# Kernel tuning notes

Hardware: AMD Instinct MI355X
Metric: run time of the kernel (lower is better)

## Reference

```python
import jax, jax.numpy as jnp
import numpy as np
import math

V, D, H, L, DFF = 32000, 1024, 16, 4, 4096
B, T_TGT, T_SRC = 4, 512, 512


def setup_inputs() -> dict:
    key = jax.random.key(0)
    ks = iter(jax.random.split(key, 64))
    s = 0.02
    inp = {
        'tgt': jax.random.randint(next(ks), (B, T_TGT), 0, V, dtype=jnp.int32),
        'encoder_output': jax.random.normal(next(ks), (B, T_SRC, D), jnp.float32),
        'tgt_mask': jnp.tril(jnp.ones((T_TGT, T_TGT), jnp.int32)),
        'emb': jax.random.normal(next(ks), (V, D)) * s,
        'Wout': jax.random.normal(next(ks), (D, V)) * s,
        'bout': jnp.zeros((V,)),
    }
    for pfx in ('s', 'c'):  # self / cross attention
        for nm in ('q', 'k', 'v', 'o'):
            inp[f'W{nm}_{pfx}'] = jax.random.normal(next(ks), (L, D, D)) * s
            inp[f'b{nm}_{pfx}'] = jnp.zeros((L, D))
    inp['W1'] = jax.random.normal(next(ks), (L, D, DFF)) * s
    inp['b1'] = jnp.zeros((L, DFF))
    inp['W2'] = jax.random.normal(next(ks), (L, DFF, D)) * s
    inp['b2'] = jnp.zeros((L, D))
    for i in (1, 2, 3):
        inp[f'ln{i}_g'] = jnp.ones((L, D))
        inp[f'ln{i}_b'] = jnp.zeros((L, D))
    return inp


def _layernorm(x, g, b, eps=1e-5):
    m = x.mean(-1, keepdims=True)
    v = ((x - m) ** 2).mean(-1, keepdims=True)
    return g * (x - m) * jax.lax.rsqrt(v + eps) + b


def _mha(xq, xkv, Wq, bq, Wk, bk, Wv, bv, Wo, bo, mask):
    Bq, Tq, Dm = xq.shape
    dk = Dm // H
    q = (xq @ Wq + bq).reshape(Bq, Tq, H, dk).transpose(0, 2, 1, 3)   # bhqd
    k = (xkv @ Wk + bk).reshape(Bq, -1, H, dk).transpose(0, 2, 1, 3)  # bhkd
    v = (xkv @ Wv + bv).reshape(Bq, -1, H, dk).transpose(0, 2, 1, 3)
    scores = jnp.einsum('bhqd,bhkd->bhqk', q, k) / math.sqrt(dk)
    if mask is not None:
        scores = jnp.where(mask[None, None] == 0, -1e9, scores)
    w = jax.nn.softmax(scores, axis=-1)                               # dropout: eval mode
    o = jnp.einsum('bhqk,bhkd->bhqd', w, v).transpose(0, 2, 1, 3).reshape(Bq, Tq, Dm)
    return o @ Wo + bo, w


def _pos_encoding(T, Dm):
    pos = jnp.arange(T, dtype=jnp.float32)[:, None]
    div = jnp.exp(jnp.arange(0, Dm, 2, dtype=jnp.float32) * (-math.log(10000.0) / Dm))
    pe = jnp.zeros((T, Dm))
    pe = pe.at[:, 0::2].set(jnp.sin(pos * div))
    pe = pe.at[:, 1::2].set(jnp.cos(pos * div))
    return pe


def reference(tgt, encoder_output, tgt_mask, emb, Wout, bout,
              Wq_s, bq_s, Wk_s, bk_s, Wv_s, bv_s, Wo_s, bo_s,
              Wq_c, bq_c, Wk_c, bk_c, Wv_c, bv_c, Wo_c, bo_c,
              W1, b1, W2, b2, ln1_g, ln1_b, ln2_g, ln2_b, ln3_g, ln3_b):
    x = emb[tgt] * math.sqrt(D) + _pos_encoding(tgt.shape[1], D)[None]
    self_ws, cross_ws = [], []
    for i in range(L):
        a1, sw = _mha(x, x, Wq_s[i], bq_s[i], Wk_s[i], bk_s[i], Wv_s[i], bv_s[i],
                      Wo_s[i], bo_s[i], tgt_mask)
        x = _layernorm(x + a1, ln1_g[i], ln1_b[i])
        a2, cw = _mha(x, encoder_output, Wq_c[i], bq_c[i], Wk_c[i], bk_c[i],
                      Wv_c[i], bv_c[i], Wo_c[i], bo_c[i], None)
        x = _layernorm(x + a2, ln2_g[i], ln2_b[i])
        ffn = jax.nn.relu(x @ W1[i] + b1[i]) @ W2[i] + b2[i]
        x = _layernorm(x + ffn, ln3_g[i], ln3_b[i])
        self_ws.append(sw)
        cross_ws.append(cw)
    logits = x @ Wout + bout
    return logits, jnp.stack(self_ws), jnp.stack(cross_ws)
```

## Files before the change

kernel.cpp:

```cpp
#include <hip/hip_runtime.h>


typedef unsigned short u16;
typedef __bf16 v8bf __attribute__((ext_vector_type(8)));
typedef float v4f __attribute__((ext_vector_type(4)));

namespace {
constexpr int kB = 4, kT = 512, kD = 1024, kH = 16, kDK = 64, kF = 4096, kV = 32000, kL = 4;
constexpr int kM = kB * kT;
constexpr long kTD = (long)kT * kD;
constexpr long kTT = (long)kT * kT;
constexpr long kHTT = (long)kH * kTT;
constexpr long kBHTT = (long)kB * kHTT;
constexpr long kLOG = (long)kM * kV;
constexpr long kPART = (long)kM * kD;
}

__device__ __forceinline__ u16 f2bf(float f) {
  union { float f; unsigned u; } v; v.f = f;
  unsigned r = v.u + 0x7FFFu + ((v.u >> 16) & 1u);
  return (u16)(r >> 16);
}
__device__ __forceinline__ float bf2f(u16 h) {
  union { unsigned u; float f; } v; v.u = ((unsigned)h) << 16;
  return v.f;
}

typedef __attribute__((address_space(3))) void lds_void;
typedef const __attribute__((address_space(1))) void glob_void;
__device__ __forceinline__ void gl2lds16(const void* g, void* l) {
  __builtin_amdgcn_global_load_lds((glob_void*)g, (lds_void*)l, 16, 0, 0);
}

template <int BM, int BN, int OUTBF, int VTR, int DBUF>
__global__ __launch_bounds__(256)
void gemm_bf(const u16* __restrict__ A0, const u16* __restrict__ B0,
             const float* __restrict__ bias, void* __restrict__ Cv,
             u16* __restrict__ vtw,
             const int K, const int lda, const int ldb, const int ldc,
             const int nH, const long sAb, const long sAh,
             const long sBb, const long sBh, const long sCb, const long sCh,
             const float scale, const int relu, const int bstride) {
  static_assert(BM % 32 == 0 && BN % 32 == 0, "tiles");
  __shared__ u16 As[DBUF + 1][BM][64];
  __shared__ u16 Bs[DBUF + 1][BN][64];
  const int tid = threadIdx.x;
  const int lane = tid & 63;
  const int w = tid >> 6;
  const int z = blockIdx.z;
  const int zb = z / nH, zh = z - zb * nH;
  const u16* A = A0 + zb * sAb + zh * sAh + (long)blockIdx.y * BM * lda;
  const u16* B = B0 + zb * sBb + zh * sBh + (long)blockIdx.x * BN * ldb;
  const long offC = zb * sCb + zh * sCh;
  const int wm = w >> 1, wn = w & 1;
  constexpr int FM = BM / 32, FN = BN / 32;
  v4f acc[FM][FN];
  const v4f zero = {0.f, 0.f, 0.f, 0.f};
#pragma unroll
  for (int i = 0; i < FM; ++i)
#pragma unroll
    for (int j = 0; j < FN; ++j) acc[i][j] = zero;
  const int l15 = lane & 15, lk = lane >> 4;
  const int lr8 = lane >> 3;
  const int swz = ((lane & 7) ^ lr8) * 8;
  const int l7 = l15 & 7;

  if constexpr (DBUF) {
#pragma unroll
    for (int s = 0; s < BM / 32; ++s)
      gl2lds16(A + (long)(w * (BM / 4) + s * 8 + lr8) * lda + swz,
               &As[0][w * (BM / 4) + s * 8][0]);
#pragma unroll
    for (int s = 0; s < BN / 32; ++s)
      gl2lds16(B + (long)(w * (BN / 4) + s * 8 + lr8) * ldb + swz,
               &Bs[0][w * (BN / 4) + s * 8][0]);

    const int NT = K >> 6;
    for (int kt = 0; kt < NT; ++kt) {
      const int cur = kt & 1;
      __syncthreads();
      if (kt + 1 < NT) {
        const int k0 = (kt + 1) << 6;
#pragma unroll
        for (int s = 0; s < BM / 32; ++s)
          gl2lds16(A + (long)(w * (BM / 4) + s * 8 + lr8) * lda + k0 + swz,
                   &As[cur ^ 1][w * (BM / 4) + s * 8][0]);
#pragma unroll
        for (int s = 0; s < BN / 32; ++s)
          gl2lds16(B + (long)(w * (BN / 4) + s * 8 + lr8) * ldb + k0 + swz,
                   &Bs[cur ^ 1][w * (BN / 4) + s * 8][0]);
      }
#pragma unroll
      for (int t = 0; t < 2; ++t) {
        const int c0 = t * 4;
        v8bf af[FM], bfr[FN];
#pragma unroll
        for (int i = 0; i < FM; ++i)
          af[i] = *(const v8bf*)&As[cur][wm * (BM / 2) + i * 16 + l15][((c0 + lk) ^ l7) * 8];
#pragma unroll
        for (int j = 0; j < FN; ++j)
          bfr[j] = *(const v8bf*)&Bs[cur][wn * (BN / 2) + j * 16 + l15][((c0 + lk) ^ l7) * 8];
#pragma unroll
        for (int i = 0; i < FM; ++i)
#pragma unroll
          for (int j = 0; j < FN; ++j)
            acc[i][j] = __builtin_amdgcn_mfma_f32_16x16x32_bf16(af[i], bfr[j], acc[i][j], 0, 0, 0);
      }
    }
  } else {
    for (int k0 = 0; k0 < K; k0 += 64) {
      __syncthreads();
#pragma unroll
      for (int s = 0; s < BM / 32; ++s)
        gl2lds16(A + (long)(w * (BM / 4) + s * 8 + lr8) * lda + k0 + swz,
                 &As[0][w * (BM / 4) + s * 8][0]);
#pragma unroll
      for (int s = 0; s < BN / 32; ++s)
        gl2lds16(B + (long)(w * (BN / 4) + s * 8 + lr8) * ldb + k0 + swz,
                 &Bs[0][w * (BN / 4) + s * 8][0]);
      __syncthreads();
#pragma unroll
      for (int t = 0; t < 2; ++t) {
        const int c0 = t * 4;
        v8bf af[FM], bfr[FN];
#pragma unroll
        for (int i = 0; i < FM; ++i)
          af[i] = *(const v8bf*)&As[0][wm * (BM / 2) + i * 16 + l15][((c0 + lk) ^ l7) * 8];
#pragma unroll
        for (int j = 0; j < FN; ++j)
          bfr[j] = *(const v8bf*)&Bs[0][wn * (BN / 2) + j * 16 + l15][((c0 + lk) ^ l7) * 8];
#pragma unroll
        for (int i = 0; i < FM; ++i)
#pragma unroll
          for (int j = 0; j < FN; ++j)
            acc[i][j] = __builtin_amdgcn_mfma_f32_16x16x32_bf16(af[i], bfr[j], acc[i][j], 0, 0, 0);
      }
    }
  }

  const long m0 = (long)blockIdx.y * BM + wm * (BM / 2);
  const int n0 = blockIdx.x * BN + wn * (BN / 2);
#pragma unroll
  for (int j = 0; j < FN; ++j) {
    const int col = n0 + j * 16 + l15;
    const float bv = (bias && zb == 0) ? bias[zh * bstride + col] : 0.0f;
#pragma unroll
    for (int i = 0; i < FM; ++i) {
      const long row = m0 + i * 16 + lk * 4;
#pragma unroll
      for (int r = 0; r < 4; ++r) {
        float v = acc[i][j][r] * scale + bv;
        if (relu) v = fmaxf(v, 0.0f);
        const long idx = offC + (row + r) * ldc + col;
        if (OUTBF) ((u16*)Cv)[idx] = f2bf(v);
        else       ((float*)Cv)[idx] = v;
        if (VTR) {
          const int colS = (int)(offC % 3072) + col;
          if (colS >= 2048) {
            const int hh = (colS - 2048) >> 6, dd = (colS - 2048) & 63;
            const int rowg = (int)(row + r);
            vtw[((long)((rowg >> 9) * 16 + hh)) * 32768 + dd * 512 + (rowg & 511)] = f2bf(v);
          }
        }
      }
    }
  }
}

template <int CAUSAL>
__global__ __launch_bounds__(512)
void attn_fused(const u16* __restrict__ Qb, const u16* __restrict__ Kb,
                const u16* __restrict__ vtp, float* __restrict__ wout,
                u16* __restrict__ oout) {
  __shared__ __align__(16) char lds[81920];
  u16 (*Qs)[64] = (u16 (*)[64])lds;
  u16 (*Ks)[64] = (u16 (*)[64])(lds + 16384);
  u16 (*Pl)[136] = (u16 (*)[136])lds;
  u16 (*Vt)[136] = (u16 (*)[136])(lds + 34816);
  __shared__ float redM[128][4];
  __shared__ float redS[128][4];
  const int tid = threadIdx.x, lane = tid & 63, w = tid >> 6;
  const int wm = w >> 2, wn = w & 3;
  const int l15 = lane & 15, lk = lane >> 4;
  const int lr8 = lane >> 3;
  const int swz = ((lane & 7) ^ lr8) * 8;
  const int l7 = l15 & 7;
  const int bx = blockIdx.x;
  const int z = blockIdx.y, zb = z >> 4, zh = z & 15;
  const u16* Q = Qb + (long)zb * 512 * 3072 + zh * 64 + (long)bx * 128 * 3072;
  const u16* Kp = Kb + (long)zb * 512 * 3072 + zh * 64;
  const u16* vtz = vtp + (long)((zb << 4) + zh) * 32768;
  const long obase = (long)zb * kHTT + (long)zh * kTT;

#pragma unroll
  for (int s = 0; s < 2; ++s)
    gl2lds16(Q + (long)(w * 16 + s * 8 + lr8) * 3072 + swz, &Qs[w * 16 + s * 8][0]);
#pragma unroll
  for (int s = 0; s < 8; ++s) {
    const int r0 = w * 64 + s * 8;
    if (!CAUSAL || r0 <= bx * 128 + 127)
      gl2lds16(Kp + (long)(r0 + lr8) * 3072 + swz, &Ks[r0][0]);
  }
  __syncthreads();

  v4f acc[4][8];
  const v4f zero = {0.f, 0.f, 0.f, 0.f};
#pragma unroll
  for (int i = 0; i < 4; ++i)
#pragma unroll
    for (int j = 0; j < 8; ++j) acc[i][j] = zero;

#pragma unroll
  for (int t = 0; t < 2; ++t) {
    const int c0 = t * 4;
    v8bf aq[4], bk[8];
#pragma unroll
    for (int i = 0; i < 4; ++i)
      aq[i] = *(const v8bf*)&Qs[wm * 64 + i * 16 + l15][((c0 + lk) ^ l7) * 8];
#pragma unroll
    for (int j = 0; j < 8; ++j)
      bk[j] = *(const v8bf*)&Ks[wn * 128 + j * 16 + l15][((c0 + lk) ^ l7) * 8];
#pragma unroll
    for (int i = 0; i < 4; ++i)
#pragma unroll
      for (int j = 0; j < 8; ++j)
        if (!(CAUSAL && wn * 128 + j * 16 > bx * 128 + wm * 64 + i * 16 + 15))
          acc[i][j] = __builtin_amdgcn_mfma_f32_16x16x32_bf16(aq[i], bk[j], acc[i][j], 0, 0, 0);
  }

  float gmax[4][4];
#pragma unroll
  for (int i = 0; i < 4; ++i)
#pragma unroll
    for (int r = 0; r < 4; ++r) {
      const int q = bx * 128 + wm * 64 + i * 16 + lk * 4 + r;
      float m = -3.0e38f;
#pragma unroll
      for (int j = 0; j < 8; ++j) {
        const int col = wn * 128 + j * 16 + l15;
        if (!CAUSAL || col <= q) m = fmaxf(m, acc[i][j][r] * 0.125f);
      }
#pragma unroll
      for (int off = 1; off < 16; off <<= 1) m = fmaxf(m, __shfl_xor(m, off));
      if (l15 == 0) redM[wm * 64 + i * 16 + lk * 4 + r][wn] = m;
    }
  __syncthreads();
#pragma unroll
  for (int i = 0; i < 4; ++i)
#pragma unroll
    for (int r = 0; r < 4; ++r) {
      v4f mv = *(const v4f*)&redM[wm * 64 + i * 16 + lk * 4 + r][0];
      gmax[i][r] = fmaxf(fmaxf(mv[0], mv[1]), fmaxf(mv[2], mv[3]));
    }
#pragma unroll
  for (int i = 0; i < 4; ++i)
#pragma unroll
    for (int r = 0; r < 4; ++r) {
      const int q = bx * 128 + wm * 64 + i * 16 + lk * 4 + r;
      float s = 0.0f;
#pragma unroll
      for (int j = 0; j < 8; ++j) {
        const int col = wn * 128 + j * 16 + l15;
        float e = (!CAUSAL || col <= q) ? __expf(acc[i][j][r] * 0.125f - gmax[i][r]) : 0.0f;
        acc[i][j][r] = e;
        s += e;
      }
#pragma unroll
      for (int off = 1; off < 16; off <<= 1) s += __shfl_xor(s, off);
      if (l15 == 0) redS[wm * 64 + i * 16 + lk * 4 + r][wn] = s;
    }
  __syncthreads();
#pragma unroll
  for (int i = 0; i < 4; ++i)
#pragma unroll
    for (int r = 0; r < 4; ++r) {
      v4f sv = *(const v4f*)&redS[wm * 64 + i * 16 + lk * 4 + r][0];
      const float inv = 1.0f / (sv[0] + sv[1] + sv[2] + sv[3]);
      const int q = bx * 128 + wm * 64 + i * 16 + lk * 4 + r;
      const long rowoff = obase + (long)q * 512;
#pragma unroll
      for (int j = 0; j < 8; ++j) {
        const int col = wn * 128 + j * 16 + l15;
        const float v = acc[i][j][r] * inv;
        acc[i][j][r] = v;
        wout[rowoff + col] = v;
      }
    }

  v4f acco[4];
#pragma unroll
  for (int i = 0; i < 4; ++i) acco[i] = zero;
  const int kcMax = CAUSAL ? bx : 3;
  for (int kc = 0; kc <= kcMax; ++kc) {
    __syncthreads();
    if (wn == kc) {
#pragma unroll
      for (int i = 0; i < 4; ++i)
#pragma unroll
        for (int j = 0; j < 8; ++j) {
          const int colk = j * 16 + l15;
#pragma unroll
          for (int r = 0; r < 4; ++r)
            Pl[wm * 64 + i * 16 + lk * 4 + r][colk] = f2bf(acc[i][j][r]);
        }
    }
#pragma unroll
    for (int s = 0; s < 2; ++s) {
      const int c = tid * 2 + s;
      const int d = c >> 4, off = (c & 15) * 8;
      uint4 vv = *(const uint4*)(vtz + (long)d * 512 + kc * 128 + off);
      *(uint4*)&Vt[d][off] = vv;
    }
    __syncthreads();
#pragma unroll
    for (int t = 0; t < 4; ++t) {
      v8bf bv = *(const v8bf*)&Vt[wn * 16 + l15][t * 32 + lk * 8];
#pragma unroll
      for (int i = 0; i < 4; ++i) {
        v8bf ap = *(const v8bf*)&Pl[wm * 64 + i * 16 + l15][t * 32 + lk * 8];
        acco[i] = __builtin_amdgcn_mfma_f32_16x16x32_bf16(ap, bv, acco[i], 0, 0, 0);
      }
    }
  }
#pragma unroll
  for (int i = 0; i < 4; ++i)
#pragma unroll
    for (int r = 0; r < 4; ++r) {
      const int row = bx * 128 + wm * 64 + i * 16 + lk * 4 + r;
      oout[(long)(zb * 512 + row) * 1024 + zh * 64 + wn * 16 + l15] = f2bf(acco[i][r]);
    }
}

struct TPtrs { const float* in[8]; u16* out[8]; };

__global__ void transpose_wt_v3(TPtrs ps, int K, int N) {
  __shared__ float tile[64][65];
  const float* in = ps.in[blockIdx.z];
  u16* o = ps.out[blockIdx.z];
  const int n0 = blockIdx.x * 64, k0 = blockIdx.y * 64;
  const int tr = threadIdx.x >> 4;
  const int tc = (threadIdx.x & 15) * 4;
#pragma unroll
  for (int i = 0; i < 4; ++i) {
    float4 v = *(const float4*)(in + (long)(k0 + tr + 16 * i) * N + n0 + tc);
    tile[tr + 16 * i][tc + 0] = v.x;
    tile[tr + 16 * i][tc + 1] = v.y;
    tile[tr + 16 * i][tc + 2] = v.z;
    tile[tr + 16 * i][tc + 3] = v.w;
  }
  __syncthreads();
#pragma unroll
  for (int i = 0; i < 4; ++i) {
    const int rr = tr + 16 * i;
    u16 h[4];
#pragma unroll
    for (int j = 0; j < 4; ++j) h[j] = f2bf(tile[tc + j][rr]);
    *(uint2*)(o + (long)(n0 + rr) * K + k0 + tc) = *(const uint2*)h;
  }
}

__global__ void concat_bias(float* __restrict__ dst, const float* __restrict__ s0,
                            const float* __restrict__ s1, const float* __restrict__ s2,
                            const int nsrc) {
  const int idx = blockIdx.x * 256 + threadIdx.x;
  const int per = nsrc << 10;
  const int l = idx / per, rem = idx - l * per, s = rem >> 10, j = rem & 1023;
  const float* src = (s == 0) ? s0 : (s == 1 ? s1 : s2);
  dst[idx] = src[l * 1024 + j];
}

__global__ void cvt_bf16_v3(const float* __restrict__ in, u16* __restrict__ o1,
                            u16* __restrict__ o2) {
  const long i = ((long)blockIdx.x * 256 + threadIdx.x) * 4;
  float4 v = *(const float4*)(in + i);
  u16 h[4] = {f2bf(v.x), f2bf(v.y), f2bf(v.z), f2bf(v.w)};
  *(uint2*)(o1 + i) = *(const uint2*)h;
  *(uint2*)(o2 + i) = *(const uint2*)h;
}

__global__ void embed_v2(const int* __restrict__ tgt, const float* __restrict__ emb,
                         float* __restrict__ x, u16* __restrict__ xb) {
  const int row = blockIdx.x;
  const int t = row & (kT - 1);
  const int tok = tgt[row];
  const int c = threadIdx.x * 4;
  float4 e = *(const float4*)(emb + (long)tok * kD + c);
  const float nl = -9.210340371976184f / (float)kD;
  const float a0 = (float)t * expf((float)c * nl);
  const float a1 = (float)t * expf((float)(c + 2) * nl);
  float4 o;
  o.x = e.x * 32.0f + sinf(a0);
  o.y = e.y * 32.0f + cosf(a0);
  o.z = e.z * 32.0f + sinf(a1);
  o.w = e.w * 32.0f + cosf(a1);
  *(float4*)(x + (long)row * kD + c) = o;
  u16 h[4] = {f2bf(o.x), f2bf(o.y), f2bf(o.z), f2bf(o.w)};
  *(uint2*)(xb + (long)row * kD + c) = *(const uint2*)h;
}

__global__ void add_ln_v3(float* __restrict__ x, u16* __restrict__ xb,
                          const float* __restrict__ res, const int nres,
                          const float* __restrict__ g, const float* __restrict__ b) {
  const int row = blockIdx.x;
  const int c = threadIdx.x * 4;
  float4 xv = *(const float4*)(x + (long)row * kD + c);
  float v0 = xv.x, v1 = xv.y, v2 = xv.z, v3 = xv.w;
  for (int p = 0; p < nres; ++p) {
    float4 rv = *(const float4*)(res + p * kPART + (long)row * kD + c);
    v0 += rv.x; v1 += rv.y; v2 += rv.z; v3 += rv.w;
  }
  float s = v0 + v1 + v2 + v3;
  float ss = v0 * v0 + v1 * v1 + v2 * v2 + v3 * v3;
#pragma unroll
  for (int o = 32; o > 0; o >>= 1) { s += __shfl_xor(s, o); ss += __shfl_xor(ss, o); }
  __shared__ float red[4][2];
  const int wv = threadIdx.x >> 6;
  if ((threadIdx.x & 63) == 0) { red[wv][0] = s; red[wv][1] = ss; }
  __syncthreads();
  s  = red[0][0] + red[1][0] + red[2][0] + red[3][0];
  ss = red[0][1] + red[1][1] + red[2][1] + red[3][1];
  const float mean = s * (1.0f / kD);
  const float var = ss * (1.0f / kD) - mean * mean;
  const float rs = rsqrtf(var + 1e-5f);
  float4 gv = *(const float4*)(g + c);
  float4 bv = *(const float4*)(b + c);
  float4 o;
  o.x = gv.x * (v0 - mean) * rs + bv.x;
  o.y = gv.y * (v1 - mean) * rs + bv.y;
  o.z = gv.z * (v2 - mean) * rs + bv.z;
  o.w = gv.w * (v3 - mean) * rs + bv.w;
  *(float4*)(x + (long)row * kD + c) = o;
  u16 h[4] = {f2bf(o.x), f2bf(o.y), f2bf(o.z), f2bf(o.w)};
  *(uint2*)(xb + (long)row * kD + c) = *(const uint2*)h;
}

template <int BM, int BN, typename TA, typename TB, int BKN>
__global__ __launch_bounds__(256)
void gemm_kernel(const void* __restrict__ Av, const void* __restrict__ Bv,
                 const float* __restrict__ bias, float* __restrict__ Cv,
                 const int K, const int lda, const int ldb, const int ldc,
                 const int nH, const long sAb, const long sAh,
                 const long sBb, const long sBh, const long sCb, const long sCh,
                 const float scale, const int relu) {
  constexpr int LP = 40;
  __shared__ u16 As[BM][LP];
  __shared__ u16 Bs[BN][LP];
  const int tid = threadIdx.x;
  const int z = blockIdx.z;
  const int zb = z / nH, zh = z - zb * nH;
  const TA* A = (const TA*)Av + zb * sAb + zh * sAh + (long)blockIdx.y * BM * lda;
  const TB* Bp;
  if constexpr (BKN)
    Bp = (const TB*)Bv + zb * sBb + zh * sBh + (long)blockIdx.x * BN;
  else
    Bp = (const TB*)Bv + zb * sBb + zh * sBh + (long)blockIdx.x * BN * ldb;
  const long offC = zb * sCb + zh * sCh;
  const int lane = tid & 63;
  const int wm = (tid >> 7) & 1, wn = (tid >> 6) & 1;
  constexpr int FM = BM / 32, FN = BN / 32;
  v4f acc[FM][FN];
  const v4f zero = {0.f, 0.f, 0.f, 0.f};
#pragma unroll
  for (int i = 0; i < FM; ++i)
#pragma unroll
    for (int j = 0; j < FN; ++j) acc[i][j] = zero;
  const int l15 = lane & 15, lk = lane >> 4;

  for (int k0 = 0; k0 < K; k0 += 32) {
    __syncthreads();
    if constexpr (sizeof(TA) == 4) {
      const int r = tid >> 3, c = (tid & 7) * 4;
#pragma unroll
      for (int rr = 0; rr < BM; rr += 32) {
        float4 vv = *(const float4*)((const float*)A + (long)(rr + r) * lda + k0 + c);
        unsigned lo = (unsigned)f2bf(vv.x) | ((unsigned)f2bf(vv.y) << 16);
        unsigned hi = (unsigned)f2bf(vv.z) | ((unsigned)f2bf(vv.w) << 16);
        *(uint2*)&As[rr + r][c] = make_uint2(lo, hi);
      }
    } else {
      const int r = tid >> 2, c = (tid & 3) * 8;
#pragma unroll
      for (int rr = 0; rr < BM; rr += 64) {
        uint4 vv = *(const uint4*)((const u16*)A + (long)(rr + r) * lda + k0 + c);
        *(uint4*)&As[rr + r][c] = vv;
      }
    }
    if constexpr (BKN) {
      const int r = tid >> 3, c = (tid & 7) * 4;
#pragma unroll
      for (int nn = 0; nn < BN; nn += 32) {
        float4 vv = *(const float4*)((const float*)Bp + (long)(k0 + r) * ldb + nn + c);
        Bs[nn + c + 0][r] = f2bf(vv.x);
        Bs[nn + c + 1][r] = f2bf(vv.y);
        Bs[nn + c + 2][r] = f2bf(vv.z);
        Bs[nn + c + 3][r] = f2bf(vv.w);
      }
    } else if constexpr (sizeof(TB) == 4) {
      const int r = tid >> 3, c = (tid & 7) * 4;
#pragma unroll
      for (int rr = 0; rr < BN; rr += 32) {
        float4 vv = *(const float4*)((const float*)Bp + (long)(rr + r) * ldb + k0 + c);
        unsigned lo = (unsigned)f2bf(vv.x) | ((unsigned)f2bf(vv.y) << 16);
        unsigned hi = (unsigned)f2bf(vv.z) | ((unsigned)f2bf(vv.w) << 16);
        *(uint2*)&Bs[rr + r][c] = make_uint2(lo, hi);
      }
    } else {
      const int r = tid >> 2, c = (tid & 3) * 8;
#pragma unroll
      for (int rr = 0; rr < BN; rr += 64) {
        uint4 vv = *(const uint4*)((const u16*)Bp + (long)(rr + r) * ldb + k0 + c);
        *(uint4*)&Bs[rr + r][c] = vv;
      }
    }
    __syncthreads();
    v8bf af[FM], bfr[FN];
#pragma unroll
    for (int i = 0; i < FM; ++i)
      af[i] = *(const v8bf*)&As[wm * (BM / 2) + i * 16 + l15][lk * 8];
#pragma unroll
    for (int j = 0; j < FN; ++j)
      bfr[j] = *(const v8bf*)&Bs[wn * (BN / 2) + j * 16 + l15][lk * 8];
#pragma unroll
    for (int i = 0; i < FM; ++i)
#pragma unroll
      for (int j = 0; j < FN; ++j)
        acc[i][j] = __builtin_amdgcn_mfma_f32_16x16x32_bf16(af[i], bfr[j], acc[i][j], 0, 0, 0);
  }

  const long m0 = (long)blockIdx.y * BM + wm * (BM / 2);
  const int n0 = blockIdx.x * BN + wn * (BN / 2);
#pragma unroll
  for (int j = 0; j < FN; ++j) {
    const int col = n0 + j * 16 + l15;
    const float bv = bias ? bias[col] : 0.0f;
#pragma unroll
    for (int i = 0; i < FM; ++i) {
      const long row = m0 + i * 16 + lk * 4;
#pragma unroll
      for (int r = 0; r < 4; ++r) {
        float v = acc[i][j][r] * scale + bv;
        if (relu) v = fmaxf(v, 0.0f);
        Cv[offC + (row + r) * ldc + col] = v;
      }
    }
  }
}

__global__ void embed_kernel(const int* __restrict__ tgt, const float* __restrict__ emb,
                             float* __restrict__ x) {
  const int row = blockIdx.x;
  const int t = row & (kT - 1);
  const int tok = tgt[row];
  const int c = threadIdx.x * 4;
  float4 e = *(const float4*)(emb + (long)tok * kD + c);
  const float nl = -9.210340371976184f / (float)kD;
  const float a0 = (float)t * expf((float)c * nl);
  const float a1 = (float)t * expf((float)(c + 2) * nl);
  float4 o;
  o.x = e.x * 32.0f + sinf(a0);
  o.y = e.y * 32.0f + cosf(a0);
  o.z = e.z * 32.0f + sinf(a1);
  o.w = e.w * 32.0f + cosf(a1);
  *(float4*)(x + (long)row * kD + c) = o;
}

__global__ void transpose_v_kernel(const float* __restrict__ v, u16* __restrict__ vt) {
  __shared__ float tile[32][33];
  const int z = blockIdx.z;
  const int b = z >> 4, h = z & 15;
  const int t0 = blockIdx.x * 32, d0 = blockIdx.y * 32;
  const int tx = threadIdx.x, ty = threadIdx.y;
  const float* in = v + (long)b * kTD + (long)h * kDK;
#pragma unroll
  for (int i = 0; i < 4; ++i)
    tile[ty + 8 * i][tx] = in[(long)(t0 + ty + 8 * i) * kD + d0 + tx];
  __syncthreads();
  u16* o = vt + (long)z * kDK * kT;
#pragma unroll
  for (int i = 0; i < 4; ++i)
    o[(long)(d0 + ty + 8 * i) * kT + t0 + tx] = f2bf(tile[tx][ty + 8 * i]);
}

__global__ void softmax_kernel(float* __restrict__ w, const int causal) {
  const int rowg = blockIdx.x * 4 + (threadIdx.x >> 6);
  const int lane = threadIdx.x & 63;
  const int q = rowg & (kT - 1);
  float* p = w + (long)rowg * kT + lane * 8;
  float4 v0 = *(const float4*)p;
  float4 v1 = *(const float4*)(p + 4);
  float f[8] = {v0.x, v0.y, v0.z, v0.w, v1.x, v1.y, v1.z, v1.w};
  const int base = lane * 8;
  float mx = -3.0e38f;
#pragma unroll
  for (int j = 0; j < 8; ++j)
    if (!causal || base + j <= q) mx = fmaxf(mx, f[j]);
#pragma unroll
  for (int o = 32; o > 0; o >>= 1) mx = fmaxf(mx, __shfl_xor(mx, o));
  float s = 0.0f;
#pragma unroll
  for (int j = 0; j < 8; ++j) {
    float e = (!causal || base + j <= q) ? __expf(f[j] - mx) : 0.0f;
    f[j] = e; s += e;
  }
#pragma unroll
  for (int o = 32; o > 0; o >>= 1) s += __shfl_xor(s, o);
  const float inv = 1.0f / s;
  float4 o0 = {f[0] * inv, f[1] * inv, f[2] * inv, f[3] * inv};
  float4 o1 = {f[4] * inv, f[5] * inv, f[6] * inv, f[7] * inv};
  *(float4*)p = o0;
  *(float4*)(p + 4) = o1;
}

__global__ void add_ln_kernel(float* __restrict__ x, const float* __restrict__ res,
                              const float* __restrict__ g, const float* __restrict__ b) {
  const int row = blockIdx.x;
  const int c = threadIdx.x * 4;
  float4 xv = *(const float4*)(x + (long)row * kD + c);
  float4 rv = *(const float4*)(res + (long)row * kD + c);
  const float v0 = xv.x + rv.x, v1 = xv.y + rv.y, v2 = xv.z + rv.z, v3 = xv.w + rv.w;
  float s = v0 + v1 + v2 + v3;
  float ss = v0 * v0 + v1 * v1 + v2 * v2 + v3 * v3;
#pragma unroll
  for (int o = 32; o > 0; o >>= 1) { s += __shfl_xor(s, o); ss += __shfl_xor(ss, o); }
  __shared__ float red[4][2];
  const int wv = threadIdx.x >> 6;
  if ((threadIdx.x & 63) == 0) { red[wv][0] = s; red[wv][1] = ss; }
  __syncthreads();
  s  = red[0][0] + red[1][0] + red[2][0] + red[3][0];
  ss = red[0][1] + red[1][1] + red[2][1] + red[3][1];
  const float mean = s * (1.0f / kD);
  const float var = ss * (1.0f / kD) - mean * mean;
  const float rs = rsqrtf(var + 1e-5f);
  float4 gv = *(const float4*)(g + c);
  float4 bv = *(const float4*)(b + c);
  float4 o;
  o.x = gv.x * (v0 - mean) * rs + bv.x;
  o.y = gv.y * (v1 - mean) * rs + bv.y;
  o.z = gv.z * (v2 - mean) * rs + bv.z;
  o.w = gv.w * (v3 - mean) * rs + bv.w;
  *(float4*)(x + (long)row * kD + c) = o;
}

extern "C" void kernel_launch(void* const* d_in, const int* in_sizes, int n_in,
                              void* d_out, int out_size, void* d_ws, size_t ws_size,
                              hipStream_t stream) {
  const int*   tgt  = (const int*)d_in[0];
  const float* enc  = (const float*)d_in[1];
  const float* emb  = (const float*)d_in[3];
  const float* Wout = (const float*)d_in[4];
  const float* bout = (const float*)d_in[5];
  const float* Wq_s = (const float*)d_in[6];
  const float* bq_s = (const float*)d_in[7];
  const float* Wk_s = (const float*)d_in[8];
  const float* bk_s = (const float*)d_in[9];
  const float* Wv_s = (const float*)d_in[10];
  const float* bv_s = (const float*)d_in[11];
  const float* Wo_s = (const float*)d_in[12];
  const float* bo_s = (const float*)d_in[13];
  const float* Wq_c = (const float*)d_in[14];
  const float* bq_c = (const float*)d_in[15];
  const float* Wk_c = (const float*)d_in[16];
  const float* bk_c = (const float*)d_in[17];
  const float* Wv_c = (const float*)d_in[18];
  const float* bv_c = (const float*)d_in[19];
  const float* Wo_c = (const float*)d_in[20];
  const float* bo_c = (const float*)d_in[21];
  const float* W1   = (const float*)d_in[22];
  const float* b1   = (const float*)d_in[23];
  const float* W2   = (const float*)d_in[24];
  const float* b2   = (const float*)d_in[25];
  const float* ln1g = (const float*)d_in[26];
  const float* ln1b = (const float*)d_in[27];
  const float* ln2g = (const float*)d_in[28];
  const float* ln2b = (const float*)d_in[29];
  const float* ln3g = (const float*)d_in[30];
  const float* ln3b = (const float*)d_in[31];

  float* out = (float*)d_out;
  const long DD = (long)kD * kD;
  const dim3 blk256(256), blkT(32, 8);

  if (ws_size >= (320ll << 20)) {
    char* ws = (char*)d_ws;
    float* x     = (float*)ws;
    u16* xb      = (u16*)(ws + (8l << 20));
    u16* encb    = (u16*)(ws + (12l << 20));
    u16* encb2   = (u16*)(ws + (16l << 20));
    u16* Sqkv    = (u16*)(ws + (20l << 20));
    u16* vt      = (u16*)(ws + (32l << 20));
    u16* S3b     = (u16*)(ws + (36l << 20));
    u16* Hb      = (u16*)(ws + (40l << 20));
    float* Spart = (float*)(ws + (56l << 20));
    u16* wbase   = (u16*)(ws + (88l << 20));
    u16* woutT   = (u16*)(ws + (216l << 20));
    float* bqkvS = (float*)(ws + (280l << 20));
    float* bqkvC = (float*)(ws + (280l << 20) + (64l << 10));
    const long WLAY = 16l * 1024 * 1024;

    for (int i = 0; i < kL; ++i) {
      u16* wqkvS = wbase + i * WLAY;
      u16* woS   = wqkvS + 3072 * 1024;
      u16* wqkvC = woS + 1024 * 1024;
      u16* woC   = wqkvC + 3072 * 1024;
      u16* w1t   = woC + 1024 * 1024;
      u16* w2t   = w1t + (long)4096 * 1024;
      TPtrs p{};
      p.in[0] = Wq_s + i * DD; p.out[0] = wqkvS;
      p.in[1] = Wk_s + i * DD; p.out[1] = wqkvS + 1024 * 1024;
      p.in[2] = Wv_s + i * DD; p.out[2] = wqkvS + 2048 * 1024;
      p.in[3] = Wo_s + i * DD; p.out[3] = woS;
      p.in[4] = Wq_c + i * DD; p.out[4] = wqkvC;
      p.in[5] = Wk_c + i * DD; p.out[5] = wqkvC + 1024 * 1024;
      p.in[6] = Wv_c + i * DD; p.out[6] = wqkvC + 2048 * 1024;
      p.in[7] = Wo_c + i * DD; p.out[7] = woC;
      transpose_wt_v3<<<dim3(16, 16, 8), blk256, 0, stream>>>(p, 1024, 1024);
      TPtrs p1{}; p1.in[0] = W1 + (long)i * kD * kF; p1.out[0] = w1t;
      transpose_wt_v3<<<dim3(64, 16, 1), blk256, 0, stream>>>(p1, 1024, 4096);
      TPtrs p2{}; p2.in[0] = W2 + (long)i * kF * kD; p2.out[0] = w2t;
      transpose_wt_v3<<<dim3(16, 64, 1), blk256, 0, stream>>>(p2, 4096, 1024);
    }
    TPtrs po{}; po.in[0] = Wout; po.out[0] = woutT;
    transpose_wt_v3<<<dim3(500, 16, 1), blk256, 0, stream>>>(po, 1024, 32000);
    concat_bias<<<dim3(48), blk256, 0, stream>>>(bqkvS, bq_s, bk_s, bv_s, 3);
    concat_bias<<<dim3(48), blk256, 0, stream>>>(bqkvC, bq_c, bk_c, bv_c, 3);
    cvt_bf16_v3<<<dim3(2048), blk256, 0, stream>>>(enc, encb, encb2);
    embed_v2<<<dim3(kM), blk256, 0, stream>>>(tgt, emb, x, xb);

    for (int i = 0; i < kL; ++i) {
      u16* wqkvS = wbase + i * WLAY;
      u16* woS   = wqkvS + 3072 * 1024;
      u16* wqkvC = woS + 1024 * 1024;
      u16* woC   = wqkvC + 3072 * 1024;
      u16* w1t   = woC + 1024 * 1024;
      u16* w2t   = w1t + (long)4096 * 1024;
      float* wSelf  = out + kLOG + (long)i * kBHTT;
      float* wCross = out + kLOG + (long)kL * kBHTT + (long)i * kBHTT;

      gemm_bf<128, 128, 1, 1, 1><<<dim3(24, 16, 1), blk256, 0, stream>>>(
          xb, wqkvS, bqkvS + i * 3072, Sqkv, vt, 1024, 1024, 1024, 3072,
          1, 0, 0, 0, 0, 0, 0, 1.0f, 0, 0);
      attn_fused<1><<<dim3(4, 64), dim3(512), 0, stream>>>(Sqkv, Sqkv + 1024, vt, wSelf, S3b);
      gemm_bf<128, 128, 0, 0, 0><<<dim3(8, 16, 4), blk256, 0, stream>>>(
          S3b, woS, bo_s + (long)i * kD, Spart, nullptr, 256, 1024, 1024, 1024,
          1, 256, 0, 256, 0, kPART, 0, 1.0f, 0, 0);
      add_ln_v3<<<dim3(kM), blk256, 0, stream>>>(x, xb, Spart, 4,
          ln1g + (long)i * kD, ln1b + (long)i * kD);

      gemm_bf<128, 128, 1, 1, 1><<<dim3(8, 16, 3), blk256, 0, stream>>>(
          xb, wqkvC, bqkvC + i * 3072, Sqkv, vt, 1024, 1024, 1024, 3072,
          3, 0, (long)2048 * 1024, 0, (long)1024 * 1024, 0, 1024, 1.0f, 0, 1024);
      attn_fused<0><<<dim3(4, 64), dim3(512), 0, stream>>>(Sqkv, Sqkv + 1024, vt, wCross, S3b);
      gemm_bf<128, 128, 0, 0, 0><<<dim3(8, 16, 4), blk256, 0, stream>>>(
          S3b, woC, bo_c + (long)i * kD, Spart, nullptr, 256, 1024, 1024, 1024,
          1, 256, 0, 256, 0, kPART, 0, 1.0f, 0, 0);
      add_ln_v3<<<dim3(kM), blk256, 0, stream>>>(x, xb, Spart, 4,
          ln2g + (long)i * kD, ln2b + (long)i * kD);

      gemm_bf<128, 128, 1, 0, 1><<<dim3(32, 16, 1), blk256, 0, stream>>>(
          xb, w1t, b1 + (long)i * kF, Hb, nullptr, 1024, 1024, 1024, 4096,
          1, 0, 0, 0, 0, 0, 0, 1.0f, 1, 0);
      gemm_bf<128, 128, 0, 0, 0><<<dim3(8, 16, 4), blk256, 0, stream>>>(
          Hb, w2t, b2 + (long)i * kD, Spart, nullptr, 1024, 4096, 4096, 1024,
          1, 1024, 0, 1024, 0, kPART, 0, 1.0f, 0, 0);
      add_ln_v3<<<dim3(kM), blk256, 0, stream>>>(x, xb, Spart, 4,
          ln3g + (long)i * kD, ln3b + (long)i * kD);
    }

    gemm_bf<128, 128, 0, 0, 1><<<dim3(250, 16, 1), blk256, 0, stream>>>(
        xb, woutT, bout, out, nullptr, 1024, 1024, 1024, 32000,
        1, 0, 0, 0, 0, 0, 0, 1.0f, 0, 0);
    return;
  }

  float* x = (float*)d_ws;
  char* sc = (char*)d_out;
  float* S0 = (float*)sc;
  float* S1 = (float*)(sc + (8l  << 20));
  float* S2 = (float*)(sc + (16l << 20));
  float* S3 = (float*)(sc + (24l << 20));
  float* S4 = (float*)(sc + (32l << 20));
  u16*   vt = (u16*)  (sc + (40l << 20));

  embed_kernel<<<dim3(kM), blk256, 0, stream>>>(tgt, emb, x);
  auto wgemm = [&](const float* A, const float* W, const float* bias, float* C) {
    gemm_kernel<128, 128, float, float, 1><<<dim3(kD / 128, kM / 128, 1), blk256, 0, stream>>>(
        A, W, bias, C, kD, kD, kD, kD, 1, 0, 0, 0, 0, 0, 0, 1.0f, 0);
  };
  for (int i = 0; i < kL; ++i) {
    const long wOff = (long)i * DD;
    float* wSelf  = out + kLOG + (long)i * kBHTT;
    float* wCross = out + kLOG + (long)kL * kBHTT + (long)i * kBHTT;
    wgemm(x, Wq_s + wOff, bq_s + (long)i * kD, S0);
    wgemm(x, Wk_s + wOff, bk_s + (long)i * kD, S1);
    wgemm(x, Wv_s + wOff, bv_s + (long)i * kD, S2);
    transpose_v_kernel<<<dim3(16, 2, 64), blkT, 0, stream>>>(S2, vt);
    gemm_kernel<128, 128, float, float, 0><<<dim3(4, 4, 64), blk256, 0, stream>>>(
        S0, S1, nullptr, wSelf, kDK, kD, kD, kT,
        kH, kTD, (long)kDK, kTD, (long)kDK, kHTT, kTT, 0.125f, 0);
    softmax_kernel<<<dim3(kB * kH * kT / 4), blk256, 0, stream>>>(wSelf, 1);
    gemm_kernel<128, 64, float, u16, 0><<<dim3(1, 4, 64), blk256, 0, stream>>>(
        wSelf, vt, nullptr, S3, kT, kT, kT, kD,
        kH, kHTT, kTT, (long)kH * kDK * kT, (long)kDK * kT, kTD, (long)kDK, 1.0f, 0);
    wgemm(S3, Wo_s + wOff, bo_s + (long)i * kD, S0);
    add_ln_kernel<<<dim3(kM), blk256, 0, stream>>>(x, S0, ln1g + (long)i * kD, ln1b + (long)i * kD);
    wgemm(x,   Wq_c + wOff, bq_c + (long)i * kD, S0);
    wgemm(enc, Wk_c + wOff, bk_c + (long)i * kD, S1);
    wgemm(enc, Wv_c + wOff, bv_c + (long)i * kD, S2);
    transpose_v_kernel<<<dim3(16, 2, 64), blkT, 0, stream>>>(S2, vt);
    gemm_kernel<128, 128, float, float, 0><<<dim3(4, 4, 64), blk256, 0, stream>>>(
        S0, S1, nullptr, wCross, kDK, kD, kD, kT,
        kH, kTD, (long)kDK, kTD, (long)kDK, kHTT, kTT, 0.125f, 0);
    softmax_kernel<<<dim3(kB * kH * kT / 4), blk256, 0, stream>>>(wCross, 0);
    gemm_kernel<128, 64, float, u16, 0><<<dim3(1, 4, 64), blk256, 0, stream>>>(
        wCross, vt, nullptr, S3, kT, kT, kT, kD,
        kH, kHTT, kTT, (long)kH * kDK * kT, (long)kDK * kT, kTD, (long)kDK, 1.0f, 0);
    wgemm(S3, Wo_c + wOff, bo_c + (long)i * kD, S0);
    add_ln_kernel<<<dim3(kM), blk256, 0, stream>>>(x, S0, ln2g + (long)i * kD, ln2b + (long)i * kD);
    gemm_kernel<128, 128, float, float, 1><<<dim3(kF / 128, kM / 128, 1), blk256, 0, stream>>>(
        x, W1 + (long)i * kD * kF, b1 + (long)i * kF, S0, kD, kD, kF, kF,
        1, 0, 0, 0, 0, 0, 0, 1.0f, 1);
    gemm_kernel<128, 128, float, float, 1><<<dim3(kD / 128, kM / 128, 1), blk256, 0, stream>>>(
        S0, W2 + (long)i * kF * kD, b2 + (long)i * kD, S4, kF, kF, kD, kD,
        1, 0, 0, 0, 0, 0, 0, 1.0f, 0);
    add_ln_kernel<<<dim3(kM), blk256, 0, stream>>>(x, S4, ln3g + (long)i * kD, ln3b + (long)i * kD);
  }
  gemm_kernel<128, 128, float, float, 1><<<dim3(kV / 128, kM / 128, 1), blk256, 0, stream>>>(
      x, Wout, bout, out, kD, kD, kV, kV,
      1, 0, 0, 0, 0, 0, 0, 1.0f, 0);
}
```

Measured before the change: 1.512 ms.

## Store split-K partials in bf16, batch weight transposes, widen logits GEMM tile

Split-K partial outputs of the output-projection and FFN-down GEMMs are now written as bf16 instead of fp32, and the add+layernorm kernel reads and widens them. This halves partial-sum traffic but rounds each partial before it is summed. The per-layer weight transposes are merged into a few launches using a 32-pointer table, which cuts launch count. The final vocab GEMM moves to a 128x256 tile with different template flags, which changes reuse and occupancy.

```diff
diff --git a/kernel.cpp b/kernel.cpp
--- a/kernel.cpp
+++ b/kernel.cpp
@@ -331,9 +331,9 @@
     }
 }
 
-struct TPtrs { const float* in[8]; u16* out[8]; };
-
-__global__ void transpose_wt_v3(TPtrs ps, int K, int N) {
+struct TPtrs32 { const float* in[32]; u16* out[32]; };
+
+__global__ void transpose_wt_v4(TPtrs32 ps, int K, int N) {
   __shared__ float tile[64][65];
   const float* in = ps.in[blockIdx.z];
   u16* o = ps.out[blockIdx.z];
@@ -398,16 +398,19 @@
   *(uint2*)(xb + (long)row * kD + c) = *(const uint2*)h;
 }
 
-__global__ void add_ln_v3(float* __restrict__ x, u16* __restrict__ xb,
-                          const float* __restrict__ res, const int nres,
+__global__ void add_ln_v4(float* __restrict__ x, u16* __restrict__ xb,
+                          const u16* __restrict__ resb, const int nres,
                           const float* __restrict__ g, const float* __restrict__ b) {
   const int row = blockIdx.x;
   const int c = threadIdx.x * 4;
   float4 xv = *(const float4*)(x + (long)row * kD + c);
   float v0 = xv.x, v1 = xv.y, v2 = xv.z, v3 = xv.w;
   for (int p = 0; p < nres; ++p) {
-    float4 rv = *(const float4*)(res + p * kPART + (long)row * kD + c);
-    v0 += rv.x; v1 += rv.y; v2 += rv.z; v3 += rv.w;
+    uint2 rv = *(const uint2*)(resb + p * kPART + (long)row * kD + c);
+    v0 += bf2f((u16)(rv.x & 0xffffu));
+    v1 += bf2f((u16)(rv.x >> 16));
+    v2 += bf2f((u16)(rv.y & 0xffffu));
+    v3 += bf2f((u16)(rv.y >> 16));
   }
   float s = v0 + v1 + v2 + v3;
   float ss = v0 * v0 + v1 * v1 + v2 * v2 + v3 * v3;
@@ -690,37 +693,45 @@
     u16* vt      = (u16*)(ws + (32l << 20));
     u16* S3b     = (u16*)(ws + (36l << 20));
     u16* Hb      = (u16*)(ws + (40l << 20));
-    float* Spart = (float*)(ws + (56l << 20));
+    u16* SpartB  = (u16*)(ws + (56l << 20));
     u16* wbase   = (u16*)(ws + (88l << 20));
     u16* woutT   = (u16*)(ws + (216l << 20));
     float* bqkvS = (float*)(ws + (280l << 20));
     float* bqkvC = (float*)(ws + (280l << 20) + (64l << 10));
     const long WLAY = 16l * 1024 * 1024;
 
-    for (int i = 0; i < kL; ++i) {
-      u16* wqkvS = wbase + i * WLAY;
-      u16* woS   = wqkvS + 3072 * 1024;
-      u16* wqkvC = woS + 1024 * 1024;
-      u16* woC   = wqkvC + 3072 * 1024;
-      u16* w1t   = woC + 1024 * 1024;
-      u16* w2t   = w1t + (long)4096 * 1024;
-      TPtrs p{};
-      p.in[0] = Wq_s + i * DD; p.out[0] = wqkvS;
-      p.in[1] = Wk_s + i * DD; p.out[1] = wqkvS + 1024 * 1024;
-      p.in[2] = Wv_s + i * DD; p.out[2] = wqkvS + 2048 * 1024;
-      p.in[3] = Wo_s + i * DD; p.out[3] = woS;
-      p.in[4] = Wq_c + i * DD; p.out[4] = wqkvC;
-      p.in[5] = Wk_c + i * DD; p.out[5] = wqkvC + 1024 * 1024;
-      p.in[6] = Wv_c + i * DD; p.out[6] = wqkvC + 2048 * 1024;
-      p.in[7] = Wo_c + i * DD; p.out[7] = woC;
-      transpose_wt_v3<<<dim3(16, 16, 8), blk256, 0, stream>>>(p, 1024, 1024);
-      TPtrs p1{}; p1.in[0] = W1 + (long)i * kD * kF; p1.out[0] = w1t;
-      transpose_wt_v3<<<dim3(64, 16, 1), blk256, 0, stream>>>(p1, 1024, 4096);
-      TPtrs p2{}; p2.in[0] = W2 + (long)i * kF * kD; p2.out[0] = w2t;
-      transpose_wt_v3<<<dim3(16, 64, 1), blk256, 0, stream>>>(p2, 4096, 1024);
-    }
-    TPtrs po{}; po.in[0] = Wout; po.out[0] = woutT;
-    transpose_wt_v3<<<dim3(500, 16, 1), blk256, 0, stream>>>(po, 1024, 32000);
+    {
+      TPtrs32 pa{};
+      for (int i = 0; i < kL; ++i) {
+        u16* wqkvS = wbase + i * WLAY;
+        u16* woS   = wqkvS + 3072 * 1024;
+        u16* wqkvC = woS + 1024 * 1024;
+        u16* woC   = wqkvC + 3072 * 1024;
+        pa.in[i * 8 + 0] = Wq_s + i * DD; pa.out[i * 8 + 0] = wqkvS;
+        pa.in[i * 8 + 1] = Wk_s + i * DD; pa.out[i * 8 + 1] = wqkvS + 1024 * 1024;
+        pa.in[i * 8 + 2] = Wv_s + i * DD; pa.out[i * 8 + 2] = wqkvS + 2048 * 1024;
+        pa.in[i * 8 + 3] = Wo_s + i * DD; pa.out[i * 8 + 3] = woS;
+        pa.in[i * 8 + 4] = Wq_c + i * DD; pa.out[i * 8 + 4] = wqkvC;
+        pa.in[i * 8 + 5] = Wk_c + i * DD; pa.out[i * 8 + 5] = wqkvC + 1024 * 1024;
+        pa.in[i * 8 + 6] = Wv_c + i * DD; pa.out[i * 8 + 6] = wqkvC + 2048 * 1024;
+        pa.in[i * 8 + 7] = Wo_c + i * DD; pa.out[i * 8 + 7] = woC;
+      }
+      transpose_wt_v4<<<dim3(16, 16, 32), blk256, 0, stream>>>(pa, 1024, 1024);
+      TPtrs32 p1{};
+      for (int i = 0; i < kL; ++i) {
+        p1.in[i] = W1 + (long)i * kD * kF;
+        p1.out[i] = wbase + i * WLAY + 8l * 1024 * 1024;
+      }
+      transpose_wt_v4<<<dim3(64, 16, 4), blk256, 0, stream>>>(p1, 1024, 4096);
+      TPtrs32 p2{};
+      for (int i = 0; i < kL; ++i) {
+        p2.in[i] = W2 + (long)i * kF * kD;
+        p2.out[i] = wbase + i * WLAY + 12l * 1024 * 1024;
+      }
+      transpose_wt_v4<<<dim3(16, 64, 4), blk256, 0, stream>>>(p2, 4096, 1024);
+      TPtrs32 po{}; po.in[0] = Wout; po.out[0] = woutT;
+      transpose_wt_v4<<<dim3(500, 16, 1), blk256, 0, stream>>>(po, 1024, 32000);
+    }
     concat_bias<<<dim3(48), blk256, 0, stream>>>(bqkvS, bq_s, bk_s, bv_s, 3);
     concat_bias<<<dim3(48), blk256, 0, stream>>>(bqkvC, bq_c, bk_c, bv_c, 3);
     cvt_bf16_v3<<<dim3(2048), blk256, 0, stream>>>(enc, encb, encb2);
@@ -740,33 +751,33 @@
           xb, wqkvS, bqkvS + i * 3072, Sqkv, vt, 1024, 1024, 1024, 3072,
           1, 0, 0, 0, 0, 0, 0, 1.0f, 0, 0);
       attn_fused<1><<<dim3(4, 64), dim3(512), 0, stream>>>(Sqkv, Sqkv + 1024, vt, wSelf, S3b);
-      gemm_bf<128, 128, 0, 0, 0><<<dim3(8, 16, 4), blk256, 0, stream>>>(
-          S3b, woS, bo_s + (long)i * kD, Spart, nullptr, 256, 1024, 1024, 1024,
+      gemm_bf<128, 128, 1, 0, 0><<<dim3(8, 16, 4), blk256, 0, stream>>>(
+          S3b, woS, bo_s + (long)i * kD, SpartB, nullptr, 256, 1024, 1024, 1024,
           1, 256, 0, 256, 0, kPART, 0, 1.0f, 0, 0);
-      add_ln_v3<<<dim3(kM), blk256, 0, stream>>>(x, xb, Spart, 4,
+      add_ln_v4<<<dim3(kM), blk256, 0, stream>>>(x, xb, SpartB, 4,
           ln1g + (long)i * kD, ln1b + (long)i * kD);
 
       gemm_bf<128, 128, 1, 1, 1><<<dim3(8, 16, 3), blk256, 0, stream>>>(
           xb, wqkvC, bqkvC + i * 3072, Sqkv, vt, 1024, 1024, 1024, 3072,
           3, 0, (long)2048 * 1024, 0, (long)1024 * 1024, 0, 1024, 1.0f, 0, 1024);
       attn_fused<0><<<dim3(4, 64), dim3(512), 0, stream>>>(Sqkv, Sqkv + 1024, vt, wCross, S3b);
-      gemm_bf<128, 128, 0, 0, 0><<<dim3(8, 16, 4), blk256, 0, stream>>>(
-          S3b, woC, bo_c + (long)i * kD, Spart, nullptr, 256, 1024, 1024, 1024,
+      gemm_bf<128, 128, 1, 0, 0><<<dim3(8, 16, 4), blk256, 0, stream>>>(
+          S3b, woC, bo_c + (long)i * kD, SpartB, nullptr, 256, 1024, 1024, 1024,
           1, 256, 0, 256, 0, kPART, 0, 1.0f, 0, 0);
-      add_ln_v3<<<dim3(kM), blk256, 0, stream>>>(x, xb, Spart, 4,
+      add_ln_v4<<<dim3(kM), blk256, 0, stream>>>(x, xb, SpartB, 4,
           ln2g + (long)i * kD, ln2b + (long)i * kD);
 
       gemm_bf<128, 128, 1, 0, 1><<<dim3(32, 16, 1), blk256, 0, stream>>>(
           xb, w1t, b1 + (long)i * kF, Hb, nullptr, 1024, 1024, 1024, 4096,
           1, 0, 0, 0, 0, 0, 0, 1.0f, 1, 0);
-      gemm_bf<128, 128, 0, 0, 0><<<dim3(8, 16, 4), blk256, 0, stream>>>(
-          Hb, w2t, b2 + (long)i * kD, Spart, nullptr, 1024, 4096, 4096, 1024,
+      gemm_bf<128, 128, 1, 0, 0><<<dim3(8, 16, 4), blk256, 0, stream>>>(
+          Hb, w2t, b2 + (long)i * kD, SpartB, nullptr, 1024, 4096, 4096, 1024,
           1, 1024, 0, 1024, 0, kPART, 0, 1.0f, 0, 0);
-      add_ln_v3<<<dim3(kM), blk256, 0, stream>>>(x, xb, Spart, 4,
+      add_ln_v4<<<dim3(kM), blk256, 0, stream>>>(x, xb, SpartB, 4,
           ln3g + (long)i * kD, ln3b + (long)i * kD);
     }
 
-    gemm_bf<128, 128, 0, 0, 1><<<dim3(250, 16, 1), blk256, 0, stream>>>(
+    gemm_bf<128, 256, 0, 0, 0><<<dim3(125, 16, 1), blk256, 0, stream>>>(
         xb, woutT, bout, out, nullptr, 1024, 1024, 1024, 32000,
         1, 0, 0, 0, 0, 0, 0, 1.0f, 0, 0);
     return;
```

After: 1.552 ms. 2.6% more time.
